# Kernel tuning notes

Measured on AMD Instinct MI355X. Metric: run time of the kernel, lower is better.

The kernel has to match this reference:

```python
import jax, jax.numpy as jnp
import numpy as np

D = 1024; NH = 16; HD = 64; FF = 4096; DEPTH = 4
P = 14; C = 3; GRID = 32; MERGE = 2; NIMG = 4
L = GRID * GRID; S = NIMG * L; ORIG = 24; EPS = 1e-6
SCALE = HD ** -0.5


def setup_inputs() -> dict:
    key = jax.random.key(0)
    ks = jax.random.split(key, 12)
    s = 0.02
    return {
        "pixel_values": jax.random.normal(ks[0], (S, C * P * P), jnp.float32),
        "grid_thw": jnp.tile(jnp.array([[1, GRID, GRID]], jnp.int32), (NIMG, 1)),
        "conv_w": jax.random.normal(ks[1], (D, C * P * P), jnp.float32) * s,
        "conv_b": jnp.zeros((D,), jnp.float32),
        "pos_embed": jax.random.normal(ks[2], (ORIG * ORIG, D), jnp.float32) * s,
        "ln1_g": jnp.ones((DEPTH, D), jnp.float32),
        "ln1_b": jnp.zeros((DEPTH, D), jnp.float32),
        "qkv_w": jax.random.normal(ks[3], (DEPTH, 3 * D, D), jnp.float32) * s,
        "qkv_b": jnp.zeros((DEPTH, 3 * D), jnp.float32),
        "proj_w": jax.random.normal(ks[4], (DEPTH, D, D), jnp.float32) * s,
        "proj_b": jnp.zeros((DEPTH, D), jnp.float32),
        "ln2_g": jnp.ones((DEPTH, D), jnp.float32),
        "ln2_b": jnp.zeros((DEPTH, D), jnp.float32),
        "fc1_w": jax.random.normal(ks[5], (DEPTH, FF, D), jnp.float32) * s,
        "fc1_b": jnp.zeros((DEPTH, FF), jnp.float32),
        "fc2_w": jax.random.normal(ks[6], (DEPTH, D, FF), jnp.float32) * s,
        "fc2_b": jnp.zeros((DEPTH, D), jnp.float32),
    }


def _pos_ids():
    # rot_pos_emb spatial-merge permutation for one t=1 image, tiled over images
    h = jnp.broadcast_to(jnp.arange(GRID)[:, None], (GRID, GRID))
    w = jnp.broadcast_to(jnp.arange(GRID)[None, :], (GRID, GRID))
    def perm(a):
        a = a.reshape(GRID // MERGE, MERGE, GRID // MERGE, MERGE)
        return a.transpose(0, 2, 1, 3).reshape(-1)
    hpos = jnp.tile(perm(h), NIMG)  # [S]
    wpos = jnp.tile(perm(w), NIMG)
    return hpos, wpos


def _bilinear_border(img, nx, ny):
    # img [H, W, D]; nx, ny in [-1, 1]; align_corners=False, padding_mode='border'
    Hh, Ww, _ = img.shape
    x = (nx + 1.0) * 0.5 * Ww - 0.5
    y = (ny + 1.0) * 0.5 * Hh - 0.5
    x0 = jnp.floor(x); y0 = jnp.floor(y)
    wx = (x - x0)[:, None]; wy = (y - y0)[:, None]
    x0i = jnp.clip(x0.astype(jnp.int32), 0, Ww - 1)
    x1i = jnp.clip(x0.astype(jnp.int32) + 1, 0, Ww - 1)
    y0i = jnp.clip(y0.astype(jnp.int32), 0, Hh - 1)
    y1i = jnp.clip(y0.astype(jnp.int32) + 1, 0, Hh - 1)
    v00 = img[y0i, x0i]; v01 = img[y0i, x1i]
    v10 = img[y1i, x0i]; v11 = img[y1i, x1i]
    return (v00 * (1 - wy) * (1 - wx) + v01 * (1 - wy) * wx
            + v10 * wy * (1 - wx) + v11 * wy * wx)


def _ln(x, g, b):
    m = jnp.mean(x, axis=-1, keepdims=True)
    v = jnp.mean(jnp.square(x - m), axis=-1, keepdims=True)
    return (x - m) * jax.lax.rsqrt(v + EPS) * g + b


def _forward(pixel_values, conv_w, conv_b, pos_embed, ln1_g, ln1_b, qkv_w, qkv_b,
             proj_w, proj_b, ln2_g, ln2_b, fc1_w, fc1_b, fc2_w, fc2_b):
    # patch embed: conv with kernel==stride==patch over one patch == linear
    x = pixel_values @ conv_w.T + conv_b  # [S, D]

    # interpolated 2D position embedding (grid_sample bilinear, border pad)
    hpos, wpos = _pos_ids()
    norm_w = (wpos.astype(jnp.float32) + 0.5) / GRID * 2.0 - 1.0
    norm_h = (hpos.astype(jnp.float32) + 0.5) / GRID * 2.0 - 1.0
    pe = _bilinear_border(pos_embed.reshape(ORIG, ORIG, D), norm_w, norm_h)
    x = x + pe

    for i in range(DEPTH):
        # attention (block-diagonal over equal-length images -> batched)
        r = x
        y = _ln(x, ln1_g[i], ln1_b[i])
        qkv = (y @ qkv_w[i].T + qkv_b[i]).reshape(NIMG, L, 3, NH, HD)
        q = qkv[:, :, 0].transpose(0, 2, 1, 3)  # [B, H, L, hd]
        k = qkv[:, :, 1].transpose(0, 2, 1, 3)
        v = qkv[:, :, 2].transpose(0, 2, 1, 3)
        scores = jnp.einsum('bhqd,bhkd->bhqk', q, k) * SCALE
        probs = jax.nn.softmax(scores, axis=-1)
        o = jnp.einsum('bhqk,bhkd->bhqd', probs, v)
        o = o.transpose(0, 2, 1, 3).reshape(S, D)
        x = r + o @ proj_w[i].T + proj_b[i]
        # MLP
        r = x
        y = _ln(x, ln2_g[i], ln2_b[i])
        h = jax.nn.gelu(y @ fc1_w[i].T + fc1_b[i], approximate=False)
        x = r + h @ fc2_w[i].T + fc2_b[i]
    return x


def reference(pixel_values, grid_thw, conv_w, conv_b, pos_embed, ln1_g, ln1_b,
              qkv_w, qkv_b, proj_w, proj_b, ln2_g, ln2_b, fc1_w, fc1_b, fc2_w, fc2_b):
    return _forward(pixel_values, conv_w, conv_b, pos_embed, ln1_g, ln1_b, qkv_w,
                    qkv_b, proj_w, proj_b, ln2_g, ln2_b, fc1_w, fc1_b, fc2_w, fc2_b)
```

## Files before the change

kernel.cpp:

```cpp
#include <hip/hip_runtime.h>
#include <math.h>

typedef __bf16 bf16x8 __attribute__((ext_vector_type(8)));
typedef float f32x4 __attribute__((ext_vector_type(4)));
typedef short s16x4 __attribute__((ext_vector_type(4)));
typedef short s16x8 __attribute__((ext_vector_type(8)));

static __device__ __forceinline__ short f2bs(float f) {
  return __builtin_bit_cast(short, (__bf16)f);
}
static __device__ __forceinline__ float bs2f(short s) {
  return __builtin_bit_cast(float, ((unsigned int)(unsigned short)s) << 16);
}

#define GLL16(gp, lp) __builtin_amdgcn_global_load_lds( \
    (const __attribute__((address_space(1))) void*)(gp), \
    (__attribute__((address_space(3))) void*)(lp), 16, 0, 0)

__global__ __launch_bounds__(256) void cvt_f32_bf16(const float* __restrict__ s,
                                                    short* __restrict__ d, int n) {
  int stride = gridDim.x * blockDim.x * 4;
  for (int j = (blockIdx.x * blockDim.x + threadIdx.x) * 4; j < n; j += stride) {
    float4 v = *(const float4*)(s + j);
    s16x4 o;
    o[0] = f2bs(v.x); o[1] = f2bs(v.y); o[2] = f2bs(v.z); o[3] = f2bs(v.w);
    *(s16x4*)(d + j) = o;
  }
}

__global__ __launch_bounds__(256) void cvt_pad(const float* __restrict__ s,
                                               short* __restrict__ d) {
  int r = blockIdx.x;
  for (int c = threadIdx.x; c < 608; c += blockDim.x)
    d[(size_t)r * 608 + c] = (c < 588) ? f2bs(s[(size_t)r * 588 + c]) : (short)0;
}

template <int N, int K, int EPI, int CM, int CN>
__global__ __launch_bounds__(256) void gemm_bt(const short* __restrict__ A,
                                               const short* __restrict__ B,
                                               const float* __restrict__ bias,
                                               const float* __restrict__ resid,
                                               void* __restrict__ out) {
  static_assert(K % 32 == 0, "K");
  constexpr int NT = K / 32;
  static_assert(NT >= 3, "pipeline depth");
  constexpr int NX = N / 128, NY = 32;
  constexpr int nwg = NX * NY;
  static_assert(nwg % 8 == 0 && (nwg / 8) % (CM * CN) == 0, "chunk");
  static_assert(NX % CN == 0 && NY % CM == 0, "cells");
  __shared__ short lA[3][128 * 32];
  __shared__ short lB[3][128 * 32];

  const int o = blockIdx.x;
  const int wid = (o & 7) * (nwg / 8) + (o >> 3);
  constexpr int cellsz = CM * CN;
  const int cell = wid / cellsz, within = wid % cellsz;
  constexpr int cellsx = NX / CN;
  const int bm0 = ((cell / cellsx) * CM + within / CN) * 128;
  const int bn0 = ((cell % cellsx) * CN + within % CN) * 128;

  const int t = threadIdx.x, w = t >> 6, lane = t & 63;
  const int wr = w >> 1, wc = w & 1;
  f32x4 acc[4][4] = {};

  const int srow = t >> 2;
  const int scol = ((t & 3) ^ ((srow >> 1) & 3)) * 8;
  const short* aP = A + (size_t)(bm0 + srow) * K + scol;
  const short* bP = B + (size_t)(bn0 + srow) * K + scol;
  const int sdst0 = (w * 16) * 32;
  const int sdst1 = (64 + w * 16) * 32;

  const int lr = lane & 15;
  const int qx = ((lane >> 4) ^ ((lr >> 1) & 3)) * 8;

  auto stage = [&](int buf, int ko) {
    GLL16(aP + ko, &lA[buf][sdst0]);
    GLL16(aP + ko + (size_t)64 * K, &lA[buf][sdst1]);
    GLL16(bP + ko, &lB[buf][sdst0]);
    GLL16(bP + ko + (size_t)64 * K, &lB[buf][sdst1]);
  };

  stage(0, 0);
  stage(1, 32);
  stage(2, 64);

  int buf = 0;
  for (int kt = 0; kt < NT; ++kt) {
    if (kt < NT - 2)       asm volatile("s_waitcnt vmcnt(8)" ::: "memory");
    else if (kt == NT - 2) asm volatile("s_waitcnt vmcnt(4)" ::: "memory");
    else                   asm volatile("s_waitcnt vmcnt(0)" ::: "memory");
    __builtin_amdgcn_s_barrier();
    asm volatile("" ::: "memory");
    __builtin_amdgcn_sched_barrier(0);

    bf16x8 af[4], bg[4];
#pragma unroll
    for (int mi = 0; mi < 4; ++mi)
      af[mi] = *(const bf16x8*)&lA[buf][(wr * 64 + mi * 16 + lr) * 32 + qx];
#pragma unroll
    for (int ni = 0; ni < 4; ++ni)
      bg[ni] = *(const bf16x8*)&lB[buf][(wc * 64 + ni * 16 + lr) * 32 + qx];

    asm volatile("s_waitcnt lgkmcnt(0)" ::: "memory");
    __builtin_amdgcn_sched_barrier(0);
    __builtin_amdgcn_s_barrier();
    asm volatile("" ::: "memory");
    __builtin_amdgcn_sched_barrier(0);

    if (kt + 3 < NT) stage(buf, (kt + 3) * 32);
    __builtin_amdgcn_sched_barrier(0);

#pragma unroll
    for (int mi = 0; mi < 4; ++mi)
#pragma unroll
      for (int ni = 0; ni < 4; ++ni)
        acc[mi][ni] = __builtin_amdgcn_mfma_f32_16x16x32_bf16(af[mi], bg[ni],
                                                              acc[mi][ni], 0, 0, 0);
    buf = (buf == 2) ? 0 : buf + 1;
  }

  const int lg4 = (lane >> 4) * 4;
#pragma unroll
  for (int mi = 0; mi < 4; ++mi) {
#pragma unroll
    for (int ni = 0; ni < 4; ++ni) {
      const int row = bm0 + wr * 64 + mi * 16 + lg4;
      const int col = bn0 + wc * 64 + ni * 16 + lr;
      const float bc = bias[col];
#pragma unroll
      for (int r = 0; r < 4; ++r) {
        float v = acc[mi][ni][r] + bc;
        size_t idx = (size_t)(row + r) * N + col;
        if constexpr (EPI == 1) v = 0.5f * v * (1.0f + erff(v * 0.70710678118f));
        if constexpr (EPI == 0 || EPI == 1) ((short*)out)[idx] = f2bs(v);
        else if constexpr (EPI == 2) ((float*)out)[idx] = v + resid[idx];
        else ((float*)out)[idx] = v;
      }
    }
  }
}

template <int N, int KC, int LDK, int EPI, int CM, int CN, int KSPLIT>
__global__ __launch_bounds__(256, 2) void gemm128(const short* __restrict__ A,
                                                  const short* __restrict__ B,
                                                  const float* __restrict__ bias,
                                                  void* __restrict__ out) {
  static_assert(KC % 64 == 0, "K");
  constexpr int NKT = KC / 64;
  static_assert(NKT >= 4 && (NKT % 2) == 0, "ktiles");
  constexpr int NX = N / 128, NY = 32;
  constexpr int nwg = NX * NY * KSPLIT;
  constexpr int cellsz = CM * CN;
  static_assert(nwg % 8 == 0 && (nwg / 8) % cellsz == 0, "chunk");
  static_assert((NX * NY) % cellsz == 0, "cellspace");
  static_assert(NX % CN == 0 && NY % CM == 0, "cells");

  __shared__ short sA[2][128 * 64];
  __shared__ short sB[2][128 * 64];

  const int o = blockIdx.x;
  const int wid = (o & 7) * (nwg / 8) + (o >> 3);
  const int kc = wid / (NX * NY);
  const int rem = wid % (NX * NY);
  const int cell = rem / cellsz, within = rem % cellsz;
  constexpr int cellsx = NX / CN;
  const int bm0 = ((cell / cellsx) * CM + within / CN) * 128;
  const int bn0 = ((cell % cellsx) * CN + within % CN) * 128;

  const int t = threadIdx.x, w = t >> 6, lane = t & 63;
  const int wr = w >> 1, wc = w & 1;
  const int lr = lane & 15, lg = lane >> 4;

  const int srow = t >> 3;
  const int sch = (t & 7) ^ (srow & 7);
  const short* aS = A + (size_t)(bm0 + srow) * LDK + kc * KC + sch * 8;
  const short* bS = B + (size_t)(bn0 + srow) * LDK + kc * KC + sch * 8;
  const int ldst = w * 512;

  auto stage = [&](int d, int kt) {
    const size_t ko = (size_t)kt * 64;
#pragma unroll
    for (int q = 0; q < 4; ++q)
      GLL16(aS + (size_t)q * 32 * LDK + ko, &sA[d][q * 2048 + ldst]);
#pragma unroll
    for (int q = 0; q < 4; ++q)
      GLL16(bS + (size_t)q * 32 * LDK + ko, &sB[d][q * 2048 + ldst]);
  };

  f32x4 acc[4][4] = {};

  stage(0, 0);
  stage(1, 1);

#define TILE(tt, dd)                                                          \
  {                                                                           \
    if ((tt) + 1 < NKT) asm volatile("s_waitcnt vmcnt(8)" ::: "memory");      \
    else                asm volatile("s_waitcnt vmcnt(0)" ::: "memory");      \
    __builtin_amdgcn_s_barrier();                                             \
    bf16x8 af[2][4], bf[2][4];                                                \
    _Pragma("unroll")                                                         \
    for (int ks = 0; ks < 2; ++ks) {                                          \
      _Pragma("unroll")                                                       \
      for (int mi = 0; mi < 4; ++mi)                                          \
        af[ks][mi] = *(const bf16x8*)&sA[dd][(wr * 64 + mi * 16 + lr) * 64 +  \
                                             (((ks << 2) + lg) ^ (lr & 7)) * 8]; \
      _Pragma("unroll")                                                       \
      for (int ni = 0; ni < 4; ++ni)                                          \
        bf[ks][ni] = *(const bf16x8*)&sB[dd][(wc * 64 + ni * 16 + lr) * 64 +  \
                                             (((ks << 2) + lg) ^ (lr & 7)) * 8]; \
    }                                                                         \
    __builtin_amdgcn_s_setprio(1);                                            \
    _Pragma("unroll")                                                         \
    for (int ks = 0; ks < 2; ++ks)                                            \
      _Pragma("unroll")                                                       \
      for (int mi = 0; mi < 4; ++mi)                                          \
        _Pragma("unroll")                                                     \
        for (int ni = 0; ni < 4; ++ni)                                        \
          acc[mi][ni] = __builtin_amdgcn_mfma_f32_16x16x32_bf16(              \
              af[ks][mi], bf[ks][ni], acc[mi][ni], 0, 0, 0);                  \
    __builtin_amdgcn_s_setprio(0);                                            \
    __builtin_amdgcn_s_barrier();                                             \
    if ((tt) + 2 < NKT) stage(dd, (tt) + 2);                                  \
  }

  for (int kt = 0; kt < NKT; kt += 2) {
    TILE(kt, 0);
    TILE(kt + 1, 1);
  }
#undef TILE

  const int lg4 = lg * 4;
#pragma unroll
  for (int mi = 0; mi < 4; ++mi) {
#pragma unroll
    for (int ni = 0; ni < 4; ++ni) {
      const int row = bm0 + wr * 64 + mi * 16 + lg4;
      const int col = bn0 + wc * 64 + ni * 16 + lr;
      float bc = 0.f;
      if constexpr (EPI != 5) bc = bias[col];
#pragma unroll
      for (int r = 0; r < 4; ++r) {
        float v = acc[mi][ni][r] + bc;
        if constexpr (EPI == 1) {
          const float u = v * (0.7978845608f + 0.0356774081f * v * v);
          v = v / (1.0f + __expf(-2.0f * u));
        }
        if constexpr (EPI == 5)
          ((short*)out)[((size_t)kc << 22) + (size_t)(row + r) * N + col] = f2bs(v);
        else
          ((short*)out)[(size_t)(row + r) * N + col] = f2bs(v);
      }
    }
  }
}

template <int N, int KC, int LDK, int EPI, int CM, int CN, int KSPLIT>
__global__ __launch_bounds__(512, 2) void gemm256(const short* __restrict__ A,
                                                  const short* __restrict__ B,
                                                  const float* __restrict__ bias,
                                                  void* __restrict__ out) {
  static_assert(KC % 64 == 0, "K");
  constexpr int NKT = KC / 64;
  static_assert(NKT >= 2, "ktiles");
  constexpr int NXT = N / 256, MYT = 16;
  constexpr int nwg = NXT * MYT * KSPLIT;
  constexpr int cellsz = CM * CN;
  static_assert(nwg % 8 == 0 && (nwg / 8) % cellsz == 0, "chunk");
  static_assert((NXT * MYT) % cellsz == 0, "cellspace");
  static_assert(NXT % CN == 0 && MYT % CM == 0, "cells");

  __shared__ short sA[2][2][8192];
  __shared__ short sB[2][2][8192];

  const int o = blockIdx.x;
  const int wid = (o & 7) * (nwg / 8) + (o >> 3);
  const int kc = wid / (NXT * MYT);
  const int rem = wid % (NXT * MYT);
  const int cell = rem / cellsz, within = rem % cellsz;
  constexpr int cellsx = NXT / CN;
  const int bm0 = ((cell / cellsx) * CM + within / CN) * 256;
  const int bn0 = ((cell % cellsx) * CN + within % CN) * 256;

  const int tid = threadIdx.x, wv = tid >> 6, lane = tid & 63;
  const int wrow = wv >> 2, wcol = wv & 3;
  const int lr = lane & 15, lg = lane >> 4;

  const int sr0 = tid >> 2;
  const int sc0 = ((tid & 3) ^ ((sr0 >> 1) & 3)) * 8;
  const short* aS0 = A + (size_t)(bm0 + sr0) * LDK + kc * KC + sc0;
  const short* bS0 = B + (size_t)(bn0 + sr0) * LDK + kc * KC + sc0;
  const int ld0 = wv * 512, ld1 = 4096 + wv * 512;

  auto stageA = [&](int d, int h, int kt) {
    const int off = kt * 64 + h * 32;
    GLL16(aS0 + off, &sA[d][h][ld0]);
    GLL16(aS0 + off + (size_t)128 * LDK, &sA[d][h][ld1]);
  };
  auto stageB = [&](int d, int h, int kt) {
    const int off = kt * 64 + h * 32;
    GLL16(bS0 + off, &sB[d][h][ld0]);
    GLL16(bS0 + off + (size_t)128 * LDK, &sB[d][h][ld1]);
  };

  const int chR = (lg ^ ((lr >> 1) & 3)) * 8;
  const int rA0 = wrow * 128 + lr;
  const int rB0 = wcol * 64 + lr;

  f32x4 acc[8][4] = {};
  bf16x8 aF[4][2], bF[4][2];

  stageA(0, 0, 0); stageA(0, 1, 0);
  stageB(0, 0, 0); stageB(0, 1, 0);
  asm volatile("s_waitcnt vmcnt(0)" ::: "memory");
  __builtin_amdgcn_s_barrier();

#define RD_A(mh)                                                              \
  _Pragma("unroll")                                                           \
  for (int f = 0; f < 4; ++f) {                                               \
    aF[f][0] = *(const bf16x8*)&sA[r][0][(rA0 + (mh)*64 + f * 16) * 32 + chR];\
    aF[f][1] = *(const bf16x8*)&sA[r][1][(rA0 + (mh)*64 + f * 16) * 32 + chR];\
  }
#define RD_B2(n0)                                                             \
  _Pragma("unroll")                                                           \
  for (int n = 0; n < 2; ++n) {                                               \
    bF[(n0)+n][0] = *(const bf16x8*)&sB[r][0][(rB0 + ((n0)+n) * 16) * 32 + chR];\
    bF[(n0)+n][1] = *(const bf16x8*)&sB[r][1][(rB0 + ((n0)+n) * 16) * 32 + chR];\
  }
#define MM(ab, n0)                                                            \
  __builtin_amdgcn_s_setprio(1);                                              \
  _Pragma("unroll")                                                           \
  for (int ks = 0; ks < 2; ++ks)                                              \
    _Pragma("unroll")                                                         \
    for (int f = 0; f < 4; ++f)                                               \
      _Pragma("unroll")                                                       \
      for (int n = 0; n < 2; ++n)                                             \
        acc[(ab)+f][(n0)+n] = __builtin_amdgcn_mfma_f32_16x16x32_bf16(        \
            aF[f][ks], bF[(n0)+n][ks], acc[(ab)+f][(n0)+n], 0, 0, 0);         \
  __builtin_amdgcn_s_setprio(0);
#define BAR __builtin_amdgcn_s_barrier();
#define LGW asm volatile("s_waitcnt lgkmcnt(0)");

  for (int t = 0; t < NKT; ++t) {
    const int r = t & 1, sd = r ^ 1;
    const bool more = (t + 1 < NKT);
    RD_A(0); RD_B2(0);
    if (more) { stageA(sd, 0, t + 1); stageA(sd, 1, t + 1); }
    BAR; LGW; MM(0, 0); BAR;
    RD_B2(2);
    if (more) { stageB(sd, 0, t + 1); stageB(sd, 1, t + 1); }
    BAR; LGW; MM(0, 2); BAR;
    RD_A(1);
    BAR; LGW; MM(4, 2); BAR;
    MM(4, 0);
    asm volatile("s_waitcnt vmcnt(0)" ::: "memory");
    BAR;
  }
#undef RD_A
#undef RD_B2
#undef MM
#undef BAR
#undef LGW

  const int lg4 = lg * 4;
#pragma unroll
  for (int mh = 0; mh < 2; ++mh) {
#pragma unroll
    for (int f = 0; f < 4; ++f) {
#pragma unroll
      for (int n = 0; n < 4; ++n) {
        const int row = bm0 + wrow * 128 + mh * 64 + f * 16 + lg4;
        const int col = bn0 + wcol * 64 + n * 16 + lr;
        float bc = 0.f;
        if constexpr (EPI != 5) bc = bias[col];
#pragma unroll
        for (int r = 0; r < 4; ++r) {
          float v = acc[mh * 4 + f][n][r] + bc;
          if constexpr (EPI == 1) {
            const float u = v * (0.7978845608f + 0.0356774081f * v * v);
            v = v / (1.0f + __expf(-2.0f * u));
          }
          if constexpr (EPI == 5)
            ((short*)out)[((size_t)kc << 22) + (size_t)(row + r) * N + col] = f2bs(v);
          else
            ((short*)out)[(size_t)(row + r) * N + col] = f2bs(v);
        }
      }
    }
  }
}

__global__ __launch_bounds__(256) void fc2_reduce(const short* __restrict__ part,
                                                  const float* __restrict__ bias,
                                                  const float* __restrict__ resid,
                                                  float* __restrict__ dest) {
  const size_t i4 = ((size_t)blockIdx.x * 256 + threadIdx.x) * 4;
  const s16x4 a0 = *(const s16x4*)(part + i4);
  const s16x4 a1 = *(const s16x4*)(part + (1ull << 22) + i4);
  const s16x4 a2 = *(const s16x4*)(part + (2ull << 22) + i4);
  const s16x4 a3 = *(const s16x4*)(part + (3ull << 22) + i4);
  const float4 rv = *(const float4*)(resid + i4);
  const float4 bv = *(const float4*)(bias + (i4 & 1023));
  float4 o;
  o.x = bs2f(a0[0]) + bs2f(a1[0]) + bs2f(a2[0]) + bs2f(a3[0]) + rv.x + bv.x;
  o.y = bs2f(a0[1]) + bs2f(a1[1]) + bs2f(a2[1]) + bs2f(a3[1]) + rv.y + bv.y;
  o.z = bs2f(a0[2]) + bs2f(a1[2]) + bs2f(a2[2]) + bs2f(a3[2]) + rv.z + bv.z;
  o.w = bs2f(a0[3]) + bs2f(a1[3]) + bs2f(a2[3]) + bs2f(a3[3]) + rv.w + bv.w;
  *(float4*)(dest + i4) = o;
}

__global__ __launch_bounds__(256) void reduce_ln(const short* __restrict__ part,
                                                 const float* __restrict__ bias,
                                                 const float* __restrict__ resid,
                                                 const float* __restrict__ g,
                                                 const float* __restrict__ b,
                                                 float* __restrict__ X,
                                                 short* __restrict__ Y) {
  const int row = blockIdx.x, t = threadIdx.x, w = t >> 6, lane = t & 63;
  const size_t i4 = (size_t)row * 1024 + t * 4;
  const s16x4 a0 = *(const s16x4*)(part + i4);
  const s16x4 a1 = *(const s16x4*)(part + (1ull << 22) + i4);
  const s16x4 a2 = *(const s16x4*)(part + (2ull << 22) + i4);
  const s16x4 a3 = *(const s16x4*)(part + (3ull << 22) + i4);
  const float4 rv = *(const float4*)(resid + i4);
  const float4 bv = *(const float4*)(bias + t * 4);
  float4 v;
  v.x = bs2f(a0[0]) + bs2f(a1[0]) + bs2f(a2[0]) + bs2f(a3[0]) + rv.x + bv.x;
  v.y = bs2f(a0[1]) + bs2f(a1[1]) + bs2f(a2[1]) + bs2f(a3[1]) + rv.y + bv.y;
  v.z = bs2f(a0[2]) + bs2f(a1[2]) + bs2f(a2[2]) + bs2f(a3[2]) + rv.z + bv.z;
  v.w = bs2f(a0[3]) + bs2f(a1[3]) + bs2f(a2[3]) + bs2f(a3[3]) + rv.w + bv.w;
  *(float4*)(X + i4) = v;

  float s = v.x + v.y + v.z + v.w;
  float ss = v.x * v.x + v.y * v.y + v.z * v.z + v.w * v.w;
#pragma unroll
  for (int m = 1; m < 64; m <<= 1) { s += __shfl_xor(s, m); ss += __shfl_xor(ss, m); }
  __shared__ float rs[4], rss[4];
  if (lane == 0) { rs[w] = s; rss[w] = ss; }
  __syncthreads();
  s = rs[0] + rs[1] + rs[2] + rs[3];
  ss = rss[0] + rss[1] + rss[2] + rss[3];
  const float mean = s * (1.f / 1024.f);
  const float var = ss * (1.f / 1024.f) - mean * mean;
  const float rstd = rsqrtf(var + 1e-6f);
  const float4 gv = ((const float4*)g)[t];
  const float4 bb = ((const float4*)b)[t];
  s16x4 o;
  o[0] = f2bs((v.x - mean) * rstd * gv.x + bb.x);
  o[1] = f2bs((v.y - mean) * rstd * gv.y + bb.y);
  o[2] = f2bs((v.z - mean) * rstd * gv.z + bb.z);
  o[3] = f2bs((v.w - mean) * rstd * gv.w + bb.w);
  *(s16x4*)(Y + i4) = o;
}

__global__ __launch_bounds__(256) void ln_fwd(const float* __restrict__ x,
                                              const float* __restrict__ g,
                                              const float* __restrict__ b,
                                              short* __restrict__ y) {
  const int row = blockIdx.x, t = threadIdx.x, w = t >> 6, lane = t & 63;
  const float4 v = ((const float4*)(x + (size_t)row * 1024))[t];
  float s = v.x + v.y + v.z + v.w;
  float ss = v.x * v.x + v.y * v.y + v.z * v.z + v.w * v.w;
#pragma unroll
  for (int m = 1; m < 64; m <<= 1) { s += __shfl_xor(s, m); ss += __shfl_xor(ss, m); }
  __shared__ float rs[4], rss[4];
  if (lane == 0) { rs[w] = s; rss[w] = ss; }
  __syncthreads();
  s = rs[0] + rs[1] + rs[2] + rs[3];
  ss = rss[0] + rss[1] + rss[2] + rss[3];
  const float mean = s * (1.f / 1024.f);
  const float var = ss * (1.f / 1024.f) - mean * mean;
  const float rstd = rsqrtf(var + 1e-6f);
  const float4 gv = ((const float4*)g)[t];
  const float4 bv = ((const float4*)b)[t];
  s16x4 o;
  o[0] = f2bs((v.x - mean) * rstd * gv.x + bv.x);
  o[1] = f2bs((v.y - mean) * rstd * gv.y + bv.y);
  o[2] = f2bs((v.z - mean) * rstd * gv.z + bv.z);
  o[3] = f2bs((v.w - mean) * rstd * gv.w + bv.w);
  *(s16x4*)(y + (size_t)row * 1024 + t * 4) = o;
}

__global__ __launch_bounds__(256) void pos_add(float* __restrict__ x,
                                               const float* __restrict__ pe) {
  const int sidx = blockIdx.x;
  const int f = sidx & 1023;
  const int wq = 2 * ((f >> 2) & 15) + (f & 1);
  const int hq = 2 * (f >> 6) + ((f >> 1) & 1);
  const float gx = (wq + 0.5f) * 0.75f - 0.5f;
  const float gy = (hq + 0.5f) * 0.75f - 0.5f;
  const float fx = floorf(gx), fy = floorf(gy);
  const float wx = gx - fx, wy = gy - fy;
  int x0 = (int)fx, y0 = (int)fy;
  const int x0i = x0 < 0 ? 0 : (x0 > 23 ? 23 : x0);
  const int x1i = (x0 + 1) < 0 ? 0 : ((x0 + 1) > 23 ? 23 : x0 + 1);
  const int y0i = y0 < 0 ? 0 : (y0 > 23 ? 23 : y0);
  const int y1i = (y0 + 1) < 0 ? 0 : ((y0 + 1) > 23 ? 23 : y0 + 1);
  const float w00 = (1 - wy) * (1 - wx), w01 = (1 - wy) * wx;
  const float w10 = wy * (1 - wx), w11 = wy * wx;
  const int c = threadIdx.x * 4;
  const float4 p00 = *(const float4*)(pe + (size_t)(y0i * 24 + x0i) * 1024 + c);
  const float4 p01 = *(const float4*)(pe + (size_t)(y0i * 24 + x1i) * 1024 + c);
  const float4 p10 = *(const float4*)(pe + (size_t)(y1i * 24 + x0i) * 1024 + c);
  const float4 p11 = *(const float4*)(pe + (size_t)(y1i * 24 + x1i) * 1024 + c);
  float* xp = x + (size_t)sidx * 1024 + c;
  float4 xv = *(float4*)xp;
  xv.x += w00 * p00.x + w01 * p01.x + w10 * p10.x + w11 * p11.x;
  xv.y += w00 * p00.y + w01 * p01.y + w10 * p10.y + w11 * p11.y;
  xv.z += w00 * p00.z + w01 * p01.z + w10 * p10.z + w11 * p11.z;
  xv.w += w00 * p00.w + w01 * p01.w + w10 * p10.w + w11 * p11.w;
  *(float4*)xp = xv;
}

__global__ __launch_bounds__(256) void attn_fwd(const short* __restrict__ qkv,
                                                short* __restrict__ outp) {
  __shared__ short lK[2][64 * 64];
  __shared__ short Vt[2][64 * 72];
  const int t = threadIdx.x, w = t >> 6, lane = t & 63;
  const int b = blockIdx.y >> 4, h = blockIdx.y & 15;
  const int sbase = b * 1024;
  const int q0 = blockIdx.x * 64 + w * 16;
  const int lr = lane & 15, lg = lane >> 4;

  const short* qrow = qkv + (size_t)(sbase + q0 + lr) * 3072 + h * 64;
  const bf16x8 qf0 = *(const bf16x8*)(qrow + lg * 8);
  const bf16x8 qf1 = *(const bf16x8*)(qrow + 32 + lg * 8);

  const int krofs = t >> 3;
  const int kcol = ((t & 7) ^ (krofs & 7)) * 8;
  const short* ksrc = qkv + (size_t)(sbase + krofs) * 3072 + 1024 + h * 64 + kcol;
  const int vkv = t >> 2, vdp = t & 3;
  const short* vsrc = qkv + (size_t)(sbase + vkv) * 3072 + 2048 + h * 64 + vdp * 16;
  const int vph = vkv ^ (vdp << 4);

  f32x4 o[4] = {};
  float psacc = 0.f;

  s16x8 v0 = *(const s16x8*)vsrc;
  s16x8 v1 = *(const s16x8*)(vsrc + 8);
  GLL16(ksrc, &lK[0][(w * 8) * 64]);
  GLL16(ksrc + (size_t)32 * 3072, &lK[0][(32 + w * 8) * 64]);
#pragma unroll
  for (int j = 0; j < 8; ++j) Vt[0][(vdp * 16 + j) * 72 + vph] = v0[j];
#pragma unroll
  for (int j = 0; j < 8; ++j) Vt[0][(vdp * 16 + 8 + j) * 72 + vph] = v1[j];
  asm volatile("s_waitcnt vmcnt(0) lgkmcnt(0)" ::: "memory");
  __builtin_amdgcn_s_barrier();

  int buf = 0;
  for (int kb = 0; kb < 16; ++kb) {
    if (kb < 15) {
      const short* vs = vsrc + (size_t)(kb + 1) * 64 * 3072;
      v0 = *(const s16x8*)vs;
      v1 = *(const s16x8*)(vs + 8);
      const short* ks = ksrc + (size_t)(kb + 1) * 64 * 3072;
      GLL16(ks, &lK[buf ^ 1][(w * 8) * 64]);
      GLL16(ks + (size_t)32 * 3072, &lK[buf ^ 1][(32 + w * 8) * 64]);
    }

    f32x4 s[4];
    __builtin_amdgcn_s_setprio(1);
#pragma unroll
    for (int sub = 0; sub < 4; ++sub) {
      const int krow = (sub * 16 + lr) * 64;
      const bf16x8 kf0 = *(const bf16x8*)&lK[buf][krow + (lg ^ (lr & 7)) * 8];
      const bf16x8 kf1 = *(const bf16x8*)&lK[buf][krow + ((lg + 4) ^ (lr & 7)) * 8];
      f32x4 a = {};
      a = __builtin_amdgcn_mfma_f32_16x16x32_bf16(kf0, qf0, a, 0, 0, 0);
      a = __builtin_amdgcn_mfma_f32_16x16x32_bf16(kf1, qf1, a, 0, 0, 0);
      s[sub] = a;
    }
    __builtin_amdgcn_s_setprio(0);

    constexpr float SC = 0.125f * 1.44269504089f;
    s16x4 pb[4];
#pragma unroll
    for (int sub = 0; sub < 4; ++sub)
#pragma unroll
      for (int r = 0; r < 4; ++r) {
        const float p = exp2f(fmaf(s[sub][r], SC, -8.0f));
        psacc += p;
        pb[sub][r] = f2bs(p);
      }

    __builtin_amdgcn_s_setprio(1);
#pragma unroll
    for (int f = 0; f < 4; ++f) {
      const int vrow = (f * 16 + lr) * 72;
#pragma unroll
      for (int sub = 0; sub < 4; ++sub) {
        const s16x4 va = *(const s16x4*)&Vt[buf][vrow + ((sub ^ f) << 4) + lg * 4];
        o[f] = __builtin_amdgcn_mfma_f32_16x16x16bf16_1k(va, pb[sub], o[f], 0, 0, 0);
      }
    }
    __builtin_amdgcn_s_setprio(0);

    if (kb < 15) {
#pragma unroll
      for (int j = 0; j < 8; ++j) Vt[buf ^ 1][(vdp * 16 + j) * 72 + vph] = v0[j];
#pragma unroll
      for (int j = 0; j < 8; ++j) Vt[buf ^ 1][(vdp * 16 + 8 + j) * 72 + vph] = v1[j];
      asm volatile("s_waitcnt vmcnt(0) lgkmcnt(0)" ::: "memory");
      __builtin_amdgcn_s_barrier();
      buf ^= 1;
    }
  }

  psacc += __shfl_xor(psacc, 16);
  psacc += __shfl_xor(psacc, 32);
  const float inv = 1.0f / psacc;
  short* orow = outp + (size_t)(sbase + q0 + lr) * 1024 + h * 64;
#pragma unroll
  for (int f = 0; f < 4; ++f) {
    s16x4 ov;
    ov[0] = f2bs(o[f][0] * inv); ov[1] = f2bs(o[f][1] * inv);
    ov[2] = f2bs(o[f][2] * inv); ov[3] = f2bs(o[f][3] * inv);
    *(s16x4*)(orow + f * 16 + lg * 4) = ov;
  }
}

extern "C" void kernel_launch(void* const* d_in, const int* in_sizes, int n_in,
                              void* d_out, int out_size, void* d_ws, size_t ws_size,
                              hipStream_t stream) {
  const float* pixel  = (const float*)d_in[0];
  const float* conv_w = (const float*)d_in[2];
  const float* conv_b = (const float*)d_in[3];
  const float* pos_e  = (const float*)d_in[4];
  const float* ln1_g  = (const float*)d_in[5];
  const float* ln1_b  = (const float*)d_in[6];
  const float* qkv_w  = (const float*)d_in[7];
  const float* qkv_b  = (const float*)d_in[8];
  const float* proj_w = (const float*)d_in[9];
  const float* proj_b = (const float*)d_in[10];
  const float* ln2_g  = (const float*)d_in[11];
  const float* ln2_b  = (const float*)d_in[12];
  const float* fc1_w  = (const float*)d_in[13];
  const float* fc1_b  = (const float*)d_in[14];
  const float* fc2_w  = (const float*)d_in[15];
  const float* fc2_b  = (const float*)d_in[16];

  char* ws = (char*)d_ws;
  short* wQKV  = (short*)(ws + 0);
  short* wPROJ = (short*)(ws + 25165824);
  short* wFC1  = (short*)(ws + 33554432);
  short* wFC2  = (short*)(ws + 67108864);
  float* X     = (float*)(ws + 100663296);
  short* Y     = (short*)(ws + 117440512);
  short* QKVB  = (short*)(ws + 125829120);
  short* ATTNO = (short*)(ws + 150994944);
  short* H     = QKVB;
  short* WPIX  = QKVB;
  short* WCONV = (short*)(ws + 125829120 + 4980736);
  short* PART  = (short*)(ws + 159383552);
  const bool wsbig = ws_size >= (size_t)159383552 + 33554432;

  cvt_f32_bf16<<<2048, 256, 0, stream>>>(qkv_w, wQKV, 4 * 3072 * 1024);
  cvt_f32_bf16<<<1024, 256, 0, stream>>>(proj_w, wPROJ, 4 * 1024 * 1024);
  cvt_f32_bf16<<<2048, 256, 0, stream>>>(fc1_w, wFC1, 4 * 4096 * 1024);
  cvt_f32_bf16<<<2048, 256, 0, stream>>>(fc2_w, wFC2, 4 * 1024 * 4096);
  cvt_pad<<<4096, 256, 0, stream>>>(pixel, WPIX);
  cvt_pad<<<1024, 256, 0, stream>>>(conv_w, WCONV);

  gemm_bt<1024, 608, 3, 4, 8><<<256, 256, 0, stream>>>(WPIX, WCONV, conv_b, nullptr, X);
  pos_add<<<4096, 256, 0, stream>>>(X, pos_e);
  ln_fwd<<<4096, 256, 0, stream>>>(X, ln1_g, ln1_b, Y);

  for (int i = 0; i < 4; ++i) {
    gemm128<3072, 1024, 1024, 0, 8, 4, 1><<<768, 256, 0, stream>>>(
        Y, wQKV + (size_t)i * 3072 * 1024, qkv_b + i * 3072, QKVB);
    attn_fwd<<<dim3(16, 64), 256, 0, stream>>>(QKVB, ATTNO);

    if (wsbig) {
      gemm128<1024, 256, 1024, 5, 8, 4, 4><<<1024, 256, 0, stream>>>(
          ATTNO, wPROJ + (size_t)i * 1024 * 1024, nullptr, PART);
      reduce_ln<<<4096, 256, 0, stream>>>(PART, proj_b + i * 1024, X,
                                          ln2_g + i * 1024, ln2_b + i * 1024, X, Y);
    } else {
      gemm_bt<1024, 1024, 2, 4, 8><<<256, 256, 0, stream>>>(
          ATTNO, wPROJ + (size_t)i * 1024 * 1024, proj_b + i * 1024, X, X);
      ln_fwd<<<4096, 256, 0, stream>>>(X, ln2_g + i * 1024, ln2_b + i * 1024, Y);
    }

    gemm256<4096, 1024, 1024, 1, 8, 4, 1><<<256, 512, 0, stream>>>(
        Y, wFC1 + (size_t)i * 4096 * 1024, fc1_b + i * 4096, H);

    if (wsbig) {
      gemm256<1024, 1024, 4096, 5, 8, 4, 4><<<256, 512, 0, stream>>>(
          H, wFC2 + (size_t)i * 1024 * 4096, nullptr, PART);
      if (i < 3) {
        reduce_ln<<<4096, 256, 0, stream>>>(PART, fc2_b + i * 1024, X,
                                            ln1_g + (i + 1) * 1024,
                                            ln1_b + (i + 1) * 1024, X, Y);
      } else {
        fc2_reduce<<<4096, 256, 0, stream>>>(PART, fc2_b + i * 1024, X,
                                             (float*)d_out);
      }
    } else {
      float* dest = (i < 3) ? X : (float*)d_out;
      gemm_bt<1024, 4096, 2, 4, 8><<<256, 256, 0, stream>>>(
          H, wFC2 + (size_t)i * 1024 * 4096, fc2_b + i * 1024, X, dest);
      if (i < 3)
        ln_fwd<<<4096, 256, 0, stream>>>(X, ln1_g + (i + 1) * 1024,
                                         ln1_b + (i + 1) * 1024, Y);
    }
  }
}
```

Measured before the change: 939.8 us.

## Process two query tiles per attention block and use 256-tile GEMM for QKV

Each attention workgroup now handles 128 query rows (two 16-row tiles per wave) against the same staged K/V tiles in LDS. This halves the number of blocks and halves the K/V global loads per query, at the cost of more registers per wave. Separately, the QKV projection switches from the 128-tile GEMM (768 blocks) to the 256-tile GEMM variant (192 blocks of 512 threads), trading parallelism for larger-tile reuse.

```diff
diff --git a/kernel.cpp b/kernel.cpp
--- a/kernel.cpp
+++ b/kernel.cpp
@@ -518,12 +518,15 @@
   const int t = threadIdx.x, w = t >> 6, lane = t & 63;
   const int b = blockIdx.y >> 4, h = blockIdx.y & 15;
   const int sbase = b * 1024;
-  const int q0 = blockIdx.x * 64 + w * 16;
+  const int q0 = blockIdx.x * 128 + w * 16;
   const int lr = lane & 15, lg = lane >> 4;
 
-  const short* qrow = qkv + (size_t)(sbase + q0 + lr) * 3072 + h * 64;
-  const bf16x8 qf0 = *(const bf16x8*)(qrow + lg * 8);
-  const bf16x8 qf1 = *(const bf16x8*)(qrow + 32 + lg * 8);
+  const short* qrowA = qkv + (size_t)(sbase + q0 + lr) * 3072 + h * 64;
+  const short* qrowB = qrowA + (size_t)64 * 3072;
+  const bf16x8 qa0 = *(const bf16x8*)(qrowA + lg * 8);
+  const bf16x8 qa1 = *(const bf16x8*)(qrowA + 32 + lg * 8);
+  const bf16x8 qb0 = *(const bf16x8*)(qrowB + lg * 8);
+  const bf16x8 qb1 = *(const bf16x8*)(qrowB + 32 + lg * 8);
 
   const int krofs = t >> 3;
   const int kcol = ((t & 7) ^ (krofs & 7)) * 8;
@@ -532,8 +535,8 @@
   const short* vsrc = qkv + (size_t)(sbase + vkv) * 3072 + 2048 + h * 64 + vdp * 16;
   const int vph = vkv ^ (vdp << 4);
 
-  f32x4 o[4] = {};
-  float psacc = 0.f;
+  f32x4 oa[4] = {}, ob[4] = {};
+  float lsA = 0.f, lsB = 0.f;
 
   s16x8 v0 = *(const s16x8*)vsrc;
   s16x8 v1 = *(const s16x8*)(vsrc + 8);
@@ -546,6 +549,7 @@
   asm volatile("s_waitcnt vmcnt(0) lgkmcnt(0)" ::: "memory");
   __builtin_amdgcn_s_barrier();
 
+  constexpr float SC = 0.125f * 1.44269504089f;
   int buf = 0;
   for (int kb = 0; kb < 16; ++kb) {
     if (kb < 15) {
@@ -557,42 +561,85 @@
       GLL16(ks + (size_t)32 * 3072, &lK[buf ^ 1][(32 + w * 8) * 64]);
     }
 
-    f32x4 s[4];
-    __builtin_amdgcn_s_setprio(1);
-#pragma unroll
-    for (int sub = 0; sub < 4; ++sub) {
-      const int krow = (sub * 16 + lr) * 64;
-      const bf16x8 kf0 = *(const bf16x8*)&lK[buf][krow + (lg ^ (lr & 7)) * 8];
-      const bf16x8 kf1 = *(const bf16x8*)&lK[buf][krow + ((lg + 4) ^ (lr & 7)) * 8];
-      f32x4 a = {};
-      a = __builtin_amdgcn_mfma_f32_16x16x32_bf16(kf0, qf0, a, 0, 0, 0);
-      a = __builtin_amdgcn_mfma_f32_16x16x32_bf16(kf1, qf1, a, 0, 0, 0);
-      s[sub] = a;
-    }
-    __builtin_amdgcn_s_setprio(0);
-
-    constexpr float SC = 0.125f * 1.44269504089f;
-    s16x4 pb[4];
-#pragma unroll
-    for (int sub = 0; sub < 4; ++sub)
-#pragma unroll
-      for (int r = 0; r < 4; ++r) {
-        const float p = exp2f(fmaf(s[sub][r], SC, -8.0f));
-        psacc += p;
-        pb[sub][r] = f2bs(p);
+    {
+      f32x4 s[4];
+      __builtin_amdgcn_s_setprio(1);
+#pragma unroll
+      for (int sub = 0; sub < 4; ++sub) {
+        const int krow = (sub * 16 + lr) * 64;
+        const bf16x8 kf0 = *(const bf16x8*)&lK[buf][krow + (lg ^ (lr & 7)) * 8];
+        const bf16x8 kf1 = *(const bf16x8*)&lK[buf][krow + ((lg + 4) ^ (lr & 7)) * 8];
+        f32x4 a = {};
+        a = __builtin_amdgcn_mfma_f32_16x16x32_bf16(kf0, qa0, a, 0, 0, 0);
+        a = __builtin_amdgcn_mfma_f32_16x16x32_bf16(kf1, qa1, a, 0, 0, 0);
+        s[sub] = a;
       }
-
-    __builtin_amdgcn_s_setprio(1);
-#pragma unroll
-    for (int f = 0; f < 4; ++f) {
-      const int vrow = (f * 16 + lr) * 72;
+      __builtin_amdgcn_s_setprio(0);
+      s16x4 pb[4];
+      float ps = 0.f;
+#pragma unroll
+      for (int sub = 0; sub < 4; ++sub)
+#pragma unroll
+        for (int r = 0; r < 4; ++r) {
+          const float p = exp2f(fmaf(s[sub][r], SC, -8.0f));
+          ps += p;
+          pb[sub][r] = f2bs(p);
+        }
+      ps += __shfl_xor(ps, 16);
+      ps += __shfl_xor(ps, 32);
+      lsA += ps;
+      __builtin_amdgcn_s_setprio(1);
+#pragma unroll
+      for (int f = 0; f < 4; ++f) {
+        const int vrow = (f * 16 + lr) * 72;
+#pragma unroll
+        for (int sub = 0; sub < 4; ++sub) {
+          const s16x4 va = *(const s16x4*)&Vt[buf][vrow + ((sub ^ f) << 4) + lg * 4];
+          oa[f] = __builtin_amdgcn_mfma_f32_16x16x16bf16_1k(va, pb[sub], oa[f], 0, 0, 0);
+        }
+      }
+      __builtin_amdgcn_s_setprio(0);
+    }
+
+    {
+      f32x4 s[4];
+      __builtin_amdgcn_s_setprio(1);
 #pragma unroll
       for (int sub = 0; sub < 4; ++sub) {
-        const s16x4 va = *(const s16x4*)&Vt[buf][vrow + ((sub ^ f) << 4) + lg * 4];
-        o[f] = __builtin_amdgcn_mfma_f32_16x16x16bf16_1k(va, pb[sub], o[f], 0, 0, 0);
+        const int krow = (sub * 16 + lr) * 64;
+        const bf16x8 kf0 = *(const bf16x8*)&lK[buf][krow + (lg ^ (lr & 7)) * 8];
+        const bf16x8 kf1 = *(const bf16x8*)&lK[buf][krow + ((lg + 4) ^ (lr & 7)) * 8];
+        f32x4 a = {};
+        a = __builtin_amdgcn_mfma_f32_16x16x32_bf16(kf0, qb0, a, 0, 0, 0);
+        a = __builtin_amdgcn_mfma_f32_16x16x32_bf16(kf1, qb1, a, 0, 0, 0);
+        s[sub] = a;
       }
-    }
-    __builtin_amdgcn_s_setprio(0);
+      __builtin_amdgcn_s_setprio(0);
+      s16x4 pb[4];
+      float ps = 0.f;
+#pragma unroll
+      for (int sub = 0; sub < 4; ++sub)
+#pragma unroll
+        for (int r = 0; r < 4; ++r) {
+          const float p = exp2f(fmaf(s[sub][r], SC, -8.0f));
+          ps += p;
+          pb[sub][r] = f2bs(p);
+        }
+      ps += __shfl_xor(ps, 16);
+      ps += __shfl_xor(ps, 32);
+      lsB += ps;
+      __builtin_amdgcn_s_setprio(1);
+#pragma unroll
+      for (int f = 0; f < 4; ++f) {
+        const int vrow = (f * 16 + lr) * 72;
+#pragma unroll
+        for (int sub = 0; sub < 4; ++sub) {
+          const s16x4 va = *(const s16x4*)&Vt[buf][vrow + ((sub ^ f) << 4) + lg * 4];
+          ob[f] = __builtin_amdgcn_mfma_f32_16x16x16bf16_1k(va, pb[sub], ob[f], 0, 0, 0);
+        }
+      }
+      __builtin_amdgcn_s_setprio(0);
+    }
 
     if (kb < 15) {
 #pragma unroll
@@ -605,16 +652,18 @@
     }
   }
 
-  psacc += __shfl_xor(psacc, 16);
-  psacc += __shfl_xor(psacc, 32);
-  const float inv = 1.0f / psacc;
-  short* orow = outp + (size_t)(sbase + q0 + lr) * 1024 + h * 64;
+  const float invA = 1.0f / lsA, invB = 1.0f / lsB;
+  short* orowA = outp + (size_t)(sbase + q0 + lr) * 1024 + h * 64;
+  short* orowB = orowA + (size_t)64 * 1024;
 #pragma unroll
   for (int f = 0; f < 4; ++f) {
     s16x4 ov;
-    ov[0] = f2bs(o[f][0] * inv); ov[1] = f2bs(o[f][1] * inv);
-    ov[2] = f2bs(o[f][2] * inv); ov[3] = f2bs(o[f][3] * inv);
-    *(s16x4*)(orow + f * 16 + lg * 4) = ov;
+    ov[0] = f2bs(oa[f][0] * invA); ov[1] = f2bs(oa[f][1] * invA);
+    ov[2] = f2bs(oa[f][2] * invA); ov[3] = f2bs(oa[f][3] * invA);
+    *(s16x4*)(orowA + f * 16 + lg * 4) = ov;
+    ov[0] = f2bs(ob[f][0] * invB); ov[1] = f2bs(ob[f][1] * invB);
+    ov[2] = f2bs(ob[f][2] * invB); ov[3] = f2bs(ob[f][3] * invB);
+    *(s16x4*)(orowB + f * 16 + lg * 4) = ov;
   }
 }
 
@@ -665,9 +714,9 @@
   ln_fwd<<<4096, 256, 0, stream>>>(X, ln1_g, ln1_b, Y);
 
   for (int i = 0; i < 4; ++i) {
-    gemm128<3072, 1024, 1024, 0, 8, 4, 1><<<768, 256, 0, stream>>>(
+    gemm256<3072, 1024, 1024, 0, 8, 3, 1><<<192, 512, 0, stream>>>(
         Y, wQKV + (size_t)i * 3072 * 1024, qkv_b + i * 3072, QKVB);
-    attn_fwd<<<dim3(16, 64), 256, 0, stream>>>(QKVB, ATTNO);
+    attn_fwd<<<dim3(8, 64), 256, 0, stream>>>(QKVB, ATTNO);
 
     if (wsbig) {
       gemm128<1024, 256, 1024, 5, 8, 4, 4><<<1024, 256, 0, stream>>>(
```

After: 935.1 us. No clear change (-0.5%).
